# Kernel tuning notes

Measured on AMD Instinct MI355X. Metric: run time of the kernel, lower is better.

## Reference

```python
import jax, jax.numpy as jnp
import numpy as np

D_MODEL = 1024
EXPANSION = 4
NUM_TILES = 4
D_FF = D_MODEL * EXPANSION


def setup_inputs() -> dict:
    key = jax.random.key(0)
    k1, k2, k3, k4, k5 = jax.random.split(key, 5)
    x = jax.random.normal(k1, (8, 2048, D_MODEL), dtype=jnp.float32)
    w_up = jax.random.normal(k2, (D_FF, D_MODEL), dtype=jnp.float32) * 0.02
    b_up = jax.random.normal(k3, (D_FF,), dtype=jnp.float32) * 0.02
    w_down = jax.random.normal(k4, (D_MODEL, D_FF), dtype=jnp.float32) * 0.02
    b_down = jax.random.normal(k5, (D_MODEL,), dtype=jnp.float32) * 0.02
    return {"x": x, "w_up": w_up, "b_up": b_up, "w_down": w_down, "b_down": b_down}


def reference(x, w_up, b_up, w_down, b_down):
    B, T, C = x.shape
    xf = x.reshape(B * T, C)  # [N, d_model]
    N = B * T

    # Emergent tile signatures: sign of per-tile row sums of up_proj weight.
    tile_up = D_FF // NUM_TILES
    signatures = jnp.sign(w_up.reshape(NUM_TILES, tile_up, C).sum(axis=1))  # [num_tiles, d_model]

    # Routing: argmax over input-signature alignment -> one-hot gate.
    scores = xf @ signatures.T                      # [N, num_tiles]
    winner = jnp.argmax(scores, axis=-1)            # [N]
    gate = jax.nn.one_hot(winner, NUM_TILES, dtype=xf.dtype)  # [N, num_tiles]

    # Tile-gated up projection (gate scales output tile blocks), then ReLU.
    hidden = xf @ w_up.T + b_up                     # [N, d_ff]
    hidden = (hidden.reshape(N, NUM_TILES, tile_up) * gate[:, :, None]).reshape(N, D_FF)
    hidden = jax.nn.relu(hidden)

    # Tile-gated down projection.
    tile_down = D_MODEL // NUM_TILES
    out = hidden @ w_down.T + b_down                # [N, d_model]
    out = (out.reshape(N, NUM_TILES, tile_down) * gate[:, :, None]).reshape(N, D_MODEL)

    return out.reshape(B, T, D_MODEL), gate.reshape(B, T, NUM_TILES)
```

## Files before the change

### kernel.cpp

```cpp
#include <hip/hip_runtime.h>
#include <stdint.h>
#include <stddef.h>

#define N_TOK 16384
#define DM    1024
#define DFF   4096
#define NT    4
#define TU    1024
#define TD    256

typedef __attribute__((ext_vector_type(8))) short  short8;
typedef __attribute__((ext_vector_type(4))) short  short4v;
typedef __attribute__((ext_vector_type(4))) float  floatx4;

__device__ inline unsigned short f2bf(float f){
  union { float f; uint32_t u; } v; v.f = f;
  uint32_t u = v.u + 0x7FFFu + ((v.u >> 16) & 1u);
  return (unsigned short)(u >> 16);
}

__device__ __forceinline__ void gll16(const void* g, void* l){
  __builtin_amdgcn_global_load_lds(
      (const __attribute__((address_space(1))) unsigned int*)g,
      (__attribute__((address_space(3))) unsigned int*)l,
      16, 0, 0);
}

__global__ void k_sig_partial(const float* __restrict__ w_up,
                              float* __restrict__ partial,
                              unsigned short* __restrict__ wupb){
  const int b = blockIdx.x, tid = threadIdx.x;
  const int tile = b >> 6, chunk = b & 63;
  const int c0 = tid * 4;
  const int row0 = tile*TU + chunk*16;
  float s0=0.f, s1=0.f, s2=0.f, s3=0.f;
  const float* base = w_up + (size_t)row0 * DM + c0;
  #pragma unroll
  for (int r = 0; r < 16; ++r){
    floatx4 v = *(const floatx4*)(base + (size_t)r * DM);
    s0 += v[0]; s1 += v[1]; s2 += v[2]; s3 += v[3];
    short4v p;
    p[0]=(short)f2bf(v[0]); p[1]=(short)f2bf(v[1]);
    p[2]=(short)f2bf(v[2]); p[3]=(short)f2bf(v[3]);
    *(short4v*)(wupb + (size_t)(row0 + r) * DM + c0) = p;
  }
  float* p = partial + ((size_t)tile*DM + c0) * 64 + chunk;
  p[0] = s0; p[64] = s1; p[128] = s2; p[192] = s3;
}

__global__ void k_sig_final(const float* __restrict__ partial,
                            float* __restrict__ sig){
  const int g = blockIdx.x * 256 + threadIdx.x;
  const float* p = partial + (size_t)g * 64;
  float s = 0.f;
  #pragma unroll
  for (int i = 0; i < 64; ++i) s += p[i];
  sig[g] = (s > 0.f) ? 1.f : ((s < 0.f) ? -1.f : 0.f);
}

__global__ void k_wdown_conv(const float* __restrict__ w,
                             unsigned short* __restrict__ wb){
  const size_t i = ((size_t)blockIdx.x * 256 + threadIdx.x) * 8;
  floatx4 v0 = *(const floatx4*)(w + i);
  floatx4 v1 = *(const floatx4*)(w + i + 4);
  short8 p;
  p[0]=(short)f2bf(v0[0]); p[1]=(short)f2bf(v0[1]); p[2]=(short)f2bf(v0[2]); p[3]=(short)f2bf(v0[3]);
  p[4]=(short)f2bf(v1[0]); p[5]=(short)f2bf(v1[1]); p[6]=(short)f2bf(v1[2]); p[7]=(short)f2bf(v1[3]);
  *(short8*)(wb + i) = p;
}

__global__ __launch_bounds__(256) void k_route(
    const float* __restrict__ x, const float* __restrict__ sig,
    float* __restrict__ gate_out, int* __restrict__ winner,
    unsigned short* __restrict__ xbf){
  __shared__ float ssig[NT * DM];
  const int tid = threadIdx.x;
  for (int i = tid; i < NT*DM; i += 256) ssig[i] = sig[i];
  __syncthreads();
  const int wv = tid >> 6, lane = tid & 63;
  const int n = blockIdx.x * 4 + wv;
  const float* xr = x + (size_t)n * DM;
  unsigned short* xb = xbf + (size_t)n * 2048 + 1024;
  double a0=0.0, a1=0.0, a2=0.0, a3=0.0;
  #pragma unroll
  for (int j = 0; j < 4; ++j){
    const int c = j*256 + lane*4;
    floatx4 v = *(const floatx4*)(xr + c);
    short4v p;
    p[0]=(short)f2bf(v[0]); p[1]=(short)f2bf(v[1]);
    p[2]=(short)f2bf(v[2]); p[3]=(short)f2bf(v[3]);
    *(short4v*)(xb + c) = p;
    #pragma unroll
    for (int u = 0; u < 4; ++u){
      double xv = (double)v[u];
      a0 += xv * (double)ssig[c+u];
      a1 += xv * (double)ssig[DM   + c+u];
      a2 += xv * (double)ssig[2*DM + c+u];
      a3 += xv * (double)ssig[3*DM + c+u];
    }
  }
  #pragma unroll
  for (int off = 32; off > 0; off >>= 1){
    a0 += __shfl_down(a0, off, 64);
    a1 += __shfl_down(a1, off, 64);
    a2 += __shfl_down(a2, off, 64);
    a3 += __shfl_down(a3, off, 64);
  }
  if (lane == 0){
    double s[4] = {a0, a1, a2, a3};
    int w = 0;
    #pragma unroll
    for (int t = 1; t < 4; ++t) if (s[t] > s[w]) w = t;
    floatx4 g = { w==0 ? 1.f:0.f, w==1 ? 1.f:0.f, w==2 ? 1.f:0.f, w==3 ? 1.f:0.f };
    *(floatx4*)(gate_out + (size_t)n * 4) = g;
    winner[n] = w;
  }
}

__global__ void k_hist(const int* __restrict__ winner,
                       int* __restrict__ blk_cnt){
  __shared__ int wcnt[4][NT];
  const int tid = threadIdx.x, wv = tid >> 6, lane = tid & 63;
  const int w = winner[blockIdx.x * 256 + tid];
  #pragma unroll
  for (int t = 0; t < NT; ++t){
    unsigned long long m = __ballot(w == t);
    if (lane == 0) wcnt[wv][t] = __popcll(m);
  }
  __syncthreads();
  if (tid < NT){
    int s = wcnt[0][tid] + wcnt[1][tid] + wcnt[2][tid] + wcnt[3][tid];
    blk_cnt[blockIdx.x * NT + tid] = s;
  }
}

__global__ void k_scan(const int* __restrict__ blk_cnt,
                       int* __restrict__ meta, int* __restrict__ blk_base){
  __shared__ int s[256];
  const int tid = threadIdx.x;
  s[tid] = blk_cnt[tid];
  __syncthreads();
  if (tid == 0){
    int tot[NT] = {0,0,0,0};
    for (int b = 0; b < 64; ++b)
      for (int t = 0; t < NT; ++t) tot[t] += s[b*NT + t];
    int off = 0, base[NT];
    for (int t = 0; t < NT; ++t){ meta[t] = tot[t]; meta[4+t] = off; base[t] = off; off += tot[t]; }
    for (int b = 0; b < 64; ++b)
      for (int t = 0; t < NT; ++t){ int c = s[b*NT + t]; s[b*NT + t] = base[t]; base[t] += c; }
  }
  __syncthreads();
  blk_base[tid] = s[tid];
}

__global__ void k_scatter(const int* __restrict__ winner,
                          const int* __restrict__ blk_base,
                          int* __restrict__ idx){
  __shared__ int wcnt[4][NT];
  const int tid = threadIdx.x, wv = tid >> 6, lane = tid & 63;
  const int n = blockIdx.x * 256 + tid;
  const int w = winner[n];
  unsigned long long mymask = 0;
  #pragma unroll
  for (int t = 0; t < NT; ++t){
    unsigned long long m = __ballot(w == t);
    if (lane == 0) wcnt[wv][t] = __popcll(m);
    if (t == w) mymask = m;
  }
  __syncthreads();
  const unsigned long long below = (lane == 0) ? 0ull : (~0ull >> (64 - lane));
  int pos = blk_base[blockIdx.x * NT + w] + __popcll(mymask & below);
  for (int v = 0; v < wv; ++v) pos += wcnt[v][w];
  idx[pos] = n;
}

__global__ __launch_bounds__(256, 2) void k_gemm1(
    const unsigned short* __restrict__ xbf,
    const unsigned short* __restrict__ wupb,
    const float* __restrict__ b_up, const int* __restrict__ meta,
    const int* __restrict__ idx, unsigned short* __restrict__ hid){
  const int tile = blockIdx.z;
  const int cnt  = meta[tile];
  const int p0   = blockIdx.x * 128;
  if (p0 >= cnt) return;
  const int off  = meta[4 + tile];
  const int nb   = blockIdx.y;

  __shared__ unsigned short smem[24576];
  __shared__ int nrow[128];

  const int tid = threadIdx.x;
  if (tid < 128){
    int p = p0 + tid;
    nrow[tid] = idx[off + (p < cnt ? p : cnt - 1)];
  }
  __syncthreads();

  const int wv = tid >> 6, lane = tid & 63;
  const int wm = (wv >> 1) * 64, wn = (wv & 1) * 64;
  const int l16 = lane & 15, quad = lane >> 4;

  const int rsub = lane >> 2;
  const int kus  = (lane & 3) * 8;

  const int ra = wv*32 + rsub;
  const unsigned short* aptr0 = xbf + (size_t)nrow[ra]      * 2048 + 1024 + kus;
  const unsigned short* aptr1 = xbf + (size_t)nrow[ra + 16] * 2048 + 1024 + kus;
  const unsigned short* bptr0 = wupb + (size_t)(tile*TU + nb*128 + wv*32 + rsub) * DM + kus;
  const unsigned short* bptr1 = bptr0 + 16 * DM;

  floatx4 acc[4][4];
  #pragma unroll
  for (int i = 0; i < 4; ++i)
    #pragma unroll
    for (int j = 0; j < 4; ++j) acc[i][j] = (floatx4){0.f,0.f,0.f,0.f};

  auto stage = [&](int b, int s){
    unsigned short* d = smem + b*8192 + wv*1024;
    const int ko = s*32;
    gll16(aptr0 + ko, d);
    gll16(aptr1 + ko, d + 512);
    gll16(bptr0 + ko, d + 4096);
    gll16(bptr1 + ko, d + 4608);
  };

  auto compute = [&](int b){
    const unsigned short* A  = smem + b*8192;
    const unsigned short* Bp = A + 4096;
    short8 af[4], bfr[4];
    #pragma unroll
    for (int i = 0; i < 4; ++i) af[i]  = *(const short8*)(A  + (wm + i*16 + l16)*32 + quad*8);
    #pragma unroll
    for (int j = 0; j < 4; ++j) bfr[j] = *(const short8*)(Bp + (wn + j*16 + l16)*32 + quad*8);
    #pragma unroll
    for (int i = 0; i < 4; ++i)
      #pragma unroll
      for (int j = 0; j < 4; ++j)
        acc[i][j] = __builtin_amdgcn_mfma_f32_16x16x32_bf16(af[i], bfr[j], acc[i][j], 0, 0, 0);
  };

  stage(0, 0);
  stage(1, 1);

  #pragma unroll
  for (int s = 0; s < 32; ++s){
    if (s == 31) asm volatile("s_waitcnt vmcnt(0)" ::: "memory");
    else         asm volatile("s_waitcnt vmcnt(4)" ::: "memory");
    __builtin_amdgcn_s_barrier();
    __builtin_amdgcn_sched_barrier(0);
    if (s < 30) stage((s + 2) % 3, s + 2);
    compute(s % 3);
    __builtin_amdgcn_sched_barrier(0);
    asm volatile("" ::: "memory");
    __builtin_amdgcn_s_barrier();
  }

  const int gcol0 = nb*128;
  #pragma unroll
  for (int half = 0; half < 2; ++half){
    if ((wv >> 1) == half){
      #pragma unroll
      for (int i = 0; i < 4; ++i){
        #pragma unroll
        for (int j = 0; j < 4; ++j){
          const int col = wn + j*16 + l16;
          const float bias = b_up[tile*TU + gcol0 + col];
          #pragma unroll
          for (int r = 0; r < 4; ++r){
            const int lrow = i*16 + quad*4 + r;
            float v = acc[i][j][r] + bias;
            smem[lrow*136 + col] = f2bf(v > 0.f ? v : 0.f);
          }
        }
      }
    }
    __syncthreads();
    #pragma unroll
    for (int c = tid; c < 1024; c += 256){
      const int lrow = c >> 4, k8 = (c & 15) * 8;
      const int m = half*64 + lrow;
      if (p0 + m < cnt){
        short8 vv = *(const short8*)(smem + lrow*136 + k8);
        *(short8*)(hid + (size_t)nrow[m]*2048 + gcol0 + k8) = vv;
      }
    }
    __syncthreads();
  }
}

__global__ __launch_bounds__(256, 2) void k_gemm2(
    const unsigned short* __restrict__ hid,
    const unsigned short* __restrict__ wdownb,
    const float* __restrict__ b_down, const int* __restrict__ meta,
    const int* __restrict__ idx, float* __restrict__ out){
  const int tile = blockIdx.z;
  const int cnt  = meta[tile];
  const int p0   = blockIdx.x * 32;
  if (p0 >= cnt) return;
  const int off  = meta[4 + tile];

  __shared__ unsigned short smem[18432];
  unsigned short* As0 = smem;
  unsigned short* As1 = smem + 1024;
  unsigned short* Bs0 = smem + 2048;
  unsigned short* Bs1 = smem + 10240;
  float* epi = (float*)smem;
  __shared__ int nrow[32];

  const int tid = threadIdx.x;
  if (tid < 32){
    int p = p0 + tid;
    nrow[tid] = idx[off + (p < cnt ? p : cnt - 1)];
  }
  __syncthreads();

  const int wv = tid >> 6, lane = tid & 63;
  const int wn = wv * 64;
  const int l16 = lane & 15, quad = lane >> 4;

  const int rsub = lane >> 2;
  const int kus  = (lane & 3) * 8;

  const int arow = (wv & 1)*16 + rsub;
  const unsigned short* aptr = hid + (size_t)nrow[arow] * 2048 + kus;
  const int aoff = (wv >> 1) * 32;
  unsigned short* asd = (wv < 2 ? As0 : As1) + ((wv & 1)*16) * 32;
  const unsigned short* bptr = wdownb + (size_t)(tile*TD + wv*64 + rsub) * DFF + tile*TU + kus;
  unsigned short* bsd0 = Bs0 + (wv*64) * 32;
  unsigned short* bsd1 = Bs1 + (wv*64) * 32;

  floatx4 acc[2][4];
  #pragma unroll
  for (int i = 0; i < 2; ++i)
    #pragma unroll
    for (int j = 0; j < 4; ++j) acc[i][j] = (floatx4){0.f,0.f,0.f,0.f};

  for (int k0 = 0; k0 < TU; k0 += 64){
    gll16(aptr + k0 + aoff, asd);
    gll16(bptr + k0,               bsd0);
    gll16(bptr + k0 + 16*DFF,      bsd0 + 16*32);
    gll16(bptr + k0 + 32*DFF,      bsd0 + 32*32);
    gll16(bptr + k0 + 48*DFF,      bsd0 + 48*32);
    gll16(bptr + k0 + 32,          bsd1);
    gll16(bptr + k0 + 32 + 16*DFF, bsd1 + 16*32);
    gll16(bptr + k0 + 32 + 32*DFF, bsd1 + 32*32);
    gll16(bptr + k0 + 32 + 48*DFF, bsd1 + 48*32);
    __syncthreads();
    {
      short8 af[2], bfr[4];
      #pragma unroll
      for (int i = 0; i < 2; ++i) af[i]  = *(const short8*)(As0 + (i*16 + l16)*32 + quad*8);
      #pragma unroll
      for (int j = 0; j < 4; ++j) bfr[j] = *(const short8*)(Bs0 + (wn + j*16 + l16)*32 + quad*8);
      #pragma unroll
      for (int i = 0; i < 2; ++i)
        #pragma unroll
        for (int j = 0; j < 4; ++j)
          acc[i][j] = __builtin_amdgcn_mfma_f32_16x16x32_bf16(af[i], bfr[j], acc[i][j], 0, 0, 0);
    }
    {
      short8 af[2], bfr[4];
      #pragma unroll
      for (int i = 0; i < 2; ++i) af[i]  = *(const short8*)(As1 + (i*16 + l16)*32 + quad*8);
      #pragma unroll
      for (int j = 0; j < 4; ++j) bfr[j] = *(const short8*)(Bs1 + (wn + j*16 + l16)*32 + quad*8);
      #pragma unroll
      for (int i = 0; i < 2; ++i)
        #pragma unroll
        for (int j = 0; j < 4; ++j)
          acc[i][j] = __builtin_amdgcn_mfma_f32_16x16x32_bf16(af[i], bfr[j], acc[i][j], 0, 0, 0);
    }
    __syncthreads();
  }

  const floatx4 z4 = {0.f, 0.f, 0.f, 0.f};
  #pragma unroll
  for (int cb = 0; cb < 4; ++cb){
    if (cb == tile) continue;
    for (int c = tid; c < 32*64; c += 256){
      const int rowl = c >> 6, c4 = (c & 63) * 4;
      if (p0 + rowl < cnt)
        *(floatx4*)(out + (size_t)nrow[rowl]*DM + cb*256 + c4) = z4;
    }
  }

  #pragma unroll
  for (int half = 0; half < 2; ++half){
    #pragma unroll
    for (int j = 0; j < 4; ++j){
      const int col = wn + j*16 + l16;
      const float bias = b_down[tile*TD + col];
      #pragma unroll
      for (int r = 0; r < 4; ++r){
        const int lrow = quad*4 + r;
        epi[lrow*260 + col] = acc[half][j][r] + bias;
      }
    }
    __syncthreads();
    #pragma unroll
    for (int c = tid; c < 1024; c += 256){
      const int lrow = c >> 6, c4 = (c & 63) * 4;
      const int m = half*16 + lrow;
      if (p0 + m < cnt){
        floatx4 v = *(const floatx4*)(epi + lrow*260 + c4);
        *(floatx4*)(out + (size_t)nrow[m]*DM + tile*TD + c4) = v;
      }
    }
    __syncthreads();
  }
}

extern "C" void kernel_launch(void* const* d_in, const int* in_sizes, int n_in,
                              void* d_out, int out_size, void* d_ws, size_t ws_size,
                              hipStream_t stream){
  const float* x      = (const float*)d_in[0];
  const float* w_up   = (const float*)d_in[1];
  const float* b_up   = (const float*)d_in[2];
  const float* w_down = (const float*)d_in[3];
  const float* b_down = (const float*)d_in[4];

  unsigned short* wupb   = (unsigned short*)d_ws;
  unsigned short* wdownb = wupb + (size_t)DFF * DM;
  float* partial = (float*)(wdownb + (size_t)DM * DFF);
  float* sig     = partial + 262144;
  int*   ints    = (int*)(sig + 4096);
  int*   winner   = ints;
  int*   idx      = ints + 16384;
  int*   meta     = ints + 32768;
  int*   blk_cnt  = ints + 32776;
  int*   blk_base = ints + 33032;

  float*          out  = (float*)d_out;
  float*          gate = out + (size_t)N_TOK * DM;
  unsigned short* ob16 = (unsigned short*)d_out;

  k_sig_partial<<<dim3(NT*64), 256, 0, stream>>>(w_up, partial, wupb);
  k_sig_final  <<<dim3(16),    256, 0, stream>>>(partial, sig);
  k_wdown_conv <<<dim3(2048),  256, 0, stream>>>(w_down, wdownb);
  k_route      <<<dim3(N_TOK/4), 256, 0, stream>>>(x, sig, gate, winner, ob16);
  k_hist       <<<dim3(64),    256, 0, stream>>>(winner, blk_cnt);
  k_scan       <<<dim3(1),     256, 0, stream>>>(blk_cnt, meta, blk_base);
  k_scatter    <<<dim3(64),    256, 0, stream>>>(winner, blk_base, idx);
  k_gemm1      <<<dim3(128, 8, NT), 256, 0, stream>>>(ob16, wupb, b_up, meta, idx, ob16);
  k_gemm2      <<<dim3(512, 1, NT), 256, 0, stream>>>(ob16, wdownb, b_down, meta, idx, out);
}
```

Baseline: 276.9 us.

## Enlarge GEMM tiles to 256x256 with 512 threads and double gemm2 row tile

Gemm1 moves from a 128x128 tile with 256 threads and a 3-stage software pipeline to a 256x256 tile with 512 threads (8 waves, 128x64 per wave), loading 64-wide K chunks per synchronous step. Gemm2 doubles its row tile from 32 to 64 tokens, so each wave holds a 4x4 accumulator and the weight tile is reused across more rows. The aim is higher arithmetic intensity and less redundant global/LDS traffic. In exchange it drops the multi-stage prefetch pipeline in gemm1, which exposes load latency, raises register pressure with 32 accumulators per wave, and produces fewer blocks, so more of the wave slots can sit idle.

Result: slower. 301.5 us (+8.9%).

```diff
diff --git a/kernel.cpp b/kernel.cpp
--- a/kernel.cpp
+++ b/kernel.cpp
@@ -174,114 +174,107 @@
   idx[pos] = n;
 }
 
-__global__ __launch_bounds__(256, 2) void k_gemm1(
+__global__ __launch_bounds__(512, 2) void k_gemm1(
     const unsigned short* __restrict__ xbf,
     const unsigned short* __restrict__ wupb,
     const float* __restrict__ b_up, const int* __restrict__ meta,
     const int* __restrict__ idx, unsigned short* __restrict__ hid){
   const int tile = blockIdx.z;
   const int cnt  = meta[tile];
-  const int p0   = blockIdx.x * 128;
+  const int p0   = blockIdx.x * 256;
   if (p0 >= cnt) return;
   const int off  = meta[4 + tile];
-  const int nb   = blockIdx.y;
-
-  __shared__ unsigned short smem[24576];
-  __shared__ int nrow[128];
+  const int nbc  = blockIdx.y * 256;
+
+  __shared__ unsigned short smem[32768];
+  __shared__ int nrow[256];
 
   const int tid = threadIdx.x;
-  if (tid < 128){
+  if (tid < 256){
     int p = p0 + tid;
     nrow[tid] = idx[off + (p < cnt ? p : cnt - 1)];
   }
   __syncthreads();
 
   const int wv = tid >> 6, lane = tid & 63;
-  const int wm = (wv >> 1) * 64, wn = (wv & 1) * 64;
+  const int wr = wv >> 2, wc = wv & 3;
   const int l16 = lane & 15, quad = lane >> 4;
-
   const int rsub = lane >> 2;
   const int kus  = (lane & 3) * 8;
 
-  const int ra = wv*32 + rsub;
-  const unsigned short* aptr0 = xbf + (size_t)nrow[ra]      * 2048 + 1024 + kus;
-  const unsigned short* aptr1 = xbf + (size_t)nrow[ra + 16] * 2048 + 1024 + kus;
-  const unsigned short* bptr0 = wupb + (size_t)(tile*TU + nb*128 + wv*32 + rsub) * DM + kus;
+  const int sr = wv*32 + rsub;
+  const unsigned short* aptr0 = xbf + (size_t)nrow[sr]      * 2048 + 1024 + kus;
+  const unsigned short* aptr1 = xbf + (size_t)nrow[sr + 16] * 2048 + 1024 + kus;
+  const unsigned short* bptr0 = wupb + (size_t)(tile*TU + nbc + wv*32 + rsub) * DM + kus;
   const unsigned short* bptr1 = bptr0 + 16 * DM;
 
-  floatx4 acc[4][4];
-  #pragma unroll
-  for (int i = 0; i < 4; ++i)
+  unsigned short* const ad0 = smem + wv*1024;
+  unsigned short* const ad1 = ad0 + 8192;
+  unsigned short* const bd0 = ad0 + 16384;
+  unsigned short* const bd1 = ad0 + 24576;
+
+  floatx4 acc[8][4];
+  #pragma unroll
+  for (int i = 0; i < 8; ++i)
     #pragma unroll
     for (int j = 0; j < 4; ++j) acc[i][j] = (floatx4){0.f,0.f,0.f,0.f};
 
-  auto stage = [&](int b, int s){
-    unsigned short* d = smem + b*8192 + wv*1024;
-    const int ko = s*32;
-    gll16(aptr0 + ko, d);
-    gll16(aptr1 + ko, d + 512);
-    gll16(bptr0 + ko, d + 4096);
-    gll16(bptr1 + ko, d + 4608);
-  };
-
-  auto compute = [&](int b){
-    const unsigned short* A  = smem + b*8192;
-    const unsigned short* Bp = A + 4096;
-    short8 af[4], bfr[4];
-    #pragma unroll
-    for (int i = 0; i < 4; ++i) af[i]  = *(const short8*)(A  + (wm + i*16 + l16)*32 + quad*8);
-    #pragma unroll
-    for (int j = 0; j < 4; ++j) bfr[j] = *(const short8*)(Bp + (wn + j*16 + l16)*32 + quad*8);
-    #pragma unroll
-    for (int i = 0; i < 4; ++i)
+  for (int k0 = 0; k0 < DM; k0 += 64){
+    gll16(aptr0 + k0,      ad0);
+    gll16(aptr1 + k0,      ad0 + 512);
+    gll16(aptr0 + k0 + 32, ad1);
+    gll16(aptr1 + k0 + 32, ad1 + 512);
+    gll16(bptr0 + k0,      bd0);
+    gll16(bptr1 + k0,      bd0 + 512);
+    gll16(bptr0 + k0 + 32, bd1);
+    gll16(bptr1 + k0 + 32, bd1 + 512);
+    __syncthreads();
+    #pragma unroll
+    for (int c = 0; c < 2; ++c){
+      const unsigned short* A  = smem + c*8192;
+      const unsigned short* Bp = smem + 16384 + c*8192;
+      short8 bfr[4];
       #pragma unroll
       for (int j = 0; j < 4; ++j)
-        acc[i][j] = __builtin_amdgcn_mfma_f32_16x16x32_bf16(af[i], bfr[j], acc[i][j], 0, 0, 0);
-  };
-
-  stage(0, 0);
-  stage(1, 1);
-
-  #pragma unroll
-  for (int s = 0; s < 32; ++s){
-    if (s == 31) asm volatile("s_waitcnt vmcnt(0)" ::: "memory");
-    else         asm volatile("s_waitcnt vmcnt(4)" ::: "memory");
-    __builtin_amdgcn_s_barrier();
-    __builtin_amdgcn_sched_barrier(0);
-    if (s < 30) stage((s + 2) % 3, s + 2);
-    compute(s % 3);
-    __builtin_amdgcn_sched_barrier(0);
-    asm volatile("" ::: "memory");
-    __builtin_amdgcn_s_barrier();
-  }
-
-  const int gcol0 = nb*128;
-  #pragma unroll
-  for (int half = 0; half < 2; ++half){
-    if ((wv >> 1) == half){
-      #pragma unroll
-      for (int i = 0; i < 4; ++i){
+        bfr[j] = *(const short8*)(Bp + (wc*64 + j*16 + l16)*32 + quad*8);
+      #pragma unroll
+      for (int i = 0; i < 8; ++i){
+        short8 af = *(const short8*)(A + (wr*128 + i*16 + l16)*32 + quad*8);
+        #pragma unroll
+        for (int j = 0; j < 4; ++j)
+          acc[i][j] = __builtin_amdgcn_mfma_f32_16x16x32_bf16(af, bfr[j], acc[i][j], 0, 0, 0);
+      }
+    }
+    __syncthreads();
+  }
+
+  #pragma unroll
+  for (int p = 0; p < 4; ++p){
+    if (wr == (p >> 1)){
+      #pragma unroll
+      for (int ii = 0; ii < 4; ++ii){
+        const int i = (p & 1)*4 + ii;
         #pragma unroll
         for (int j = 0; j < 4; ++j){
-          const int col = wn + j*16 + l16;
-          const float bias = b_up[tile*TU + gcol0 + col];
+          const int col = wc*64 + j*16 + l16;
+          const float bias = b_up[tile*TU + nbc + col];
           #pragma unroll
           for (int r = 0; r < 4; ++r){
-            const int lrow = i*16 + quad*4 + r;
+            const int lrow = ii*16 + quad*4 + r;
             float v = acc[i][j][r] + bias;
-            smem[lrow*136 + col] = f2bf(v > 0.f ? v : 0.f);
+            smem[lrow*264 + col] = f2bf(v > 0.f ? v : 0.f);
           }
         }
       }
     }
     __syncthreads();
     #pragma unroll
-    for (int c = tid; c < 1024; c += 256){
-      const int lrow = c >> 4, k8 = (c & 15) * 8;
-      const int m = half*64 + lrow;
+    for (int c = tid; c < 2048; c += 512){
+      const int lrow = c >> 5, k8 = (c & 31) * 8;
+      const int m = p*64 + lrow;
       if (p0 + m < cnt){
-        short8 vv = *(const short8*)(smem + lrow*136 + k8);
-        *(short8*)(hid + (size_t)nrow[m]*2048 + gcol0 + k8) = vv;
+        short8 vv = *(const short8*)(smem + lrow*264 + k8);
+        *(short8*)(hid + (size_t)nrow[m]*2048 + nbc + k8) = vv;
       }
     }
     __syncthreads();
@@ -295,20 +288,16 @@
     const int* __restrict__ idx, float* __restrict__ out){
   const int tile = blockIdx.z;
   const int cnt  = meta[tile];
-  const int p0   = blockIdx.x * 32;
+  const int p0   = blockIdx.x * 64;
   if (p0 >= cnt) return;
   const int off  = meta[4 + tile];
 
-  __shared__ unsigned short smem[18432];
-  unsigned short* As0 = smem;
-  unsigned short* As1 = smem + 1024;
-  unsigned short* Bs0 = smem + 2048;
-  unsigned short* Bs1 = smem + 10240;
+  __shared__ unsigned short smem[20480];
   float* epi = (float*)smem;
-  __shared__ int nrow[32];
+  __shared__ int nrow[64];
 
   const int tid = threadIdx.x;
-  if (tid < 32){
+  if (tid < 64){
     int p = p0 + tid;
     nrow[tid] = idx[off + (p < cnt ? p : cnt - 1)];
   }
@@ -317,59 +306,49 @@
   const int wv = tid >> 6, lane = tid & 63;
   const int wn = wv * 64;
   const int l16 = lane & 15, quad = lane >> 4;
-
   const int rsub = lane >> 2;
   const int kus  = (lane & 3) * 8;
 
-  const int arow = (wv & 1)*16 + rsub;
-  const unsigned short* aptr = hid + (size_t)nrow[arow] * 2048 + kus;
-  const int aoff = (wv >> 1) * 32;
-  unsigned short* asd = (wv < 2 ? As0 : As1) + ((wv & 1)*16) * 32;
+  const unsigned short* aptr = hid + (size_t)nrow[wv*16 + rsub] * 2048 + kus;
+  unsigned short* const asd0 = smem + (wv*16) * 32;
+  unsigned short* const asd1 = asd0 + 2048;
   const unsigned short* bptr = wdownb + (size_t)(tile*TD + wv*64 + rsub) * DFF + tile*TU + kus;
-  unsigned short* bsd0 = Bs0 + (wv*64) * 32;
-  unsigned short* bsd1 = Bs1 + (wv*64) * 32;
-
-  floatx4 acc[2][4];
-  #pragma unroll
-  for (int i = 0; i < 2; ++i)
+  unsigned short* const bsd0 = smem + 4096  + (wv*64) * 32;
+  unsigned short* const bsd1 = bsd0 + 8192;
+
+  floatx4 acc[4][4];
+  #pragma unroll
+  for (int i = 0; i < 4; ++i)
     #pragma unroll
     for (int j = 0; j < 4; ++j) acc[i][j] = (floatx4){0.f,0.f,0.f,0.f};
 
   for (int k0 = 0; k0 < TU; k0 += 64){
-    gll16(aptr + k0 + aoff, asd);
+    gll16(aptr + k0,      asd0);
+    gll16(aptr + k0 + 32, asd1);
     gll16(bptr + k0,               bsd0);
-    gll16(bptr + k0 + 16*DFF,      bsd0 + 16*32);
-    gll16(bptr + k0 + 32*DFF,      bsd0 + 32*32);
-    gll16(bptr + k0 + 48*DFF,      bsd0 + 48*32);
+    gll16(bptr + k0 + 16*DFF,      bsd0 + 512);
+    gll16(bptr + k0 + 32*DFF,      bsd0 + 1024);
+    gll16(bptr + k0 + 48*DFF,      bsd0 + 1536);
     gll16(bptr + k0 + 32,          bsd1);
-    gll16(bptr + k0 + 32 + 16*DFF, bsd1 + 16*32);
-    gll16(bptr + k0 + 32 + 32*DFF, bsd1 + 32*32);
-    gll16(bptr + k0 + 32 + 48*DFF, bsd1 + 48*32);
-    __syncthreads();
-    {
-      short8 af[2], bfr[4];
-      #pragma unroll
-      for (int i = 0; i < 2; ++i) af[i]  = *(const short8*)(As0 + (i*16 + l16)*32 + quad*8);
-      #pragma unroll
-      for (int j = 0; j < 4; ++j) bfr[j] = *(const short8*)(Bs0 + (wn + j*16 + l16)*32 + quad*8);
-      #pragma unroll
-      for (int i = 0; i < 2; ++i)
+    gll16(bptr + k0 + 32 + 16*DFF, bsd1 + 512);
+    gll16(bptr + k0 + 32 + 32*DFF, bsd1 + 1024);
+    gll16(bptr + k0 + 32 + 48*DFF, bsd1 + 1536);
+    __syncthreads();
+    #pragma unroll
+    for (int c = 0; c < 2; ++c){
+      const unsigned short* A  = smem + c*2048;
+      const unsigned short* Bp = smem + 4096 + c*8192;
+      short8 af[4], bfr[4];
+      #pragma unroll
+      for (int i = 0; i < 4; ++i) af[i]  = *(const short8*)(A  + (i*16 + l16)*32 + quad*8);
+      #pragma unroll
+      for (int j = 0; j < 4; ++j) bfr[j] = *(const short8*)(Bp + (wn + j*16 + l16)*32 + quad*8);
+      #pragma unroll
+      for (int i = 0; i < 4; ++i)
         #pragma unroll
         for (int j = 0; j < 4; ++j)
           acc[i][j] = __builtin_amdgcn_mfma_f32_16x16x32_bf16(af[i], bfr[j], acc[i][j], 0, 0, 0);
     }
-    {
-      short8 af[2], bfr[4];
-      #pragma unroll
-      for (int i = 0; i < 2; ++i) af[i]  = *(const short8*)(As1 + (i*16 + l16)*32 + quad*8);
-      #pragma unroll
-      for (int j = 0; j < 4; ++j) bfr[j] = *(const short8*)(Bs1 + (wn + j*16 + l16)*32 + quad*8);
-      #pragma unroll
-      for (int i = 0; i < 2; ++i)
-        #pragma unroll
-        for (int j = 0; j < 4; ++j)
-          acc[i][j] = __builtin_amdgcn_mfma_f32_16x16x32_bf16(af[i], bfr[j], acc[i][j], 0, 0, 0);
-    }
     __syncthreads();
   }
 
@@ -377,7 +356,7 @@
   #pragma unroll
   for (int cb = 0; cb < 4; ++cb){
     if (cb == tile) continue;
-    for (int c = tid; c < 32*64; c += 256){
+    for (int c = tid; c < 64*64; c += 256){
       const int rowl = c >> 6, c4 = (c & 63) * 4;
       if (p0 + rowl < cnt)
         *(floatx4*)(out + (size_t)nrow[rowl]*DM + cb*256 + c4) = z4;
@@ -385,22 +364,26 @@
   }
 
   #pragma unroll
-  for (int half = 0; half < 2; ++half){
-    #pragma unroll
-    for (int j = 0; j < 4; ++j){
-      const int col = wn + j*16 + l16;
-      const float bias = b_down[tile*TD + col];
-      #pragma unroll
-      for (int r = 0; r < 4; ++r){
-        const int lrow = quad*4 + r;
-        epi[lrow*260 + col] = acc[half][j][r] + bias;
+  for (int h = 0; h < 2; ++h){
+    #pragma unroll
+    for (int ii = 0; ii < 2; ++ii){
+      const int i = h*2 + ii;
+      #pragma unroll
+      for (int j = 0; j < 4; ++j){
+        const int col = wn + j*16 + l16;
+        const float bias = b_down[tile*TD + col];
+        #pragma unroll
+        for (int r = 0; r < 4; ++r){
+          const int lrow = ii*16 + quad*4 + r;
+          epi[lrow*260 + col] = acc[i][j][r] + bias;
+        }
       }
     }
     __syncthreads();
     #pragma unroll
-    for (int c = tid; c < 1024; c += 256){
+    for (int c = tid; c < 2048; c += 256){
       const int lrow = c >> 6, c4 = (c & 63) * 4;
-      const int m = half*16 + lrow;
+      const int m = h*32 + lrow;
       if (p0 + m < cnt){
         floatx4 v = *(const floatx4*)(epi + lrow*260 + c4);
         *(floatx4*)(out + (size_t)nrow[m]*DM + tile*TD + c4) = v;
@@ -441,6 +424,6 @@
   k_hist       <<<dim3(64),    256, 0, stream>>>(winner, blk_cnt);
   k_scan       <<<dim3(1),     256, 0, stream>>>(blk_cnt, meta, blk_base);
   k_scatter    <<<dim3(64),    256, 0, stream>>>(winner, blk_base, idx);
-  k_gemm1      <<<dim3(128, 8, NT), 256, 0, stream>>>(ob16, wupb, b_up, meta, idx, ob16);
-  k_gemm2      <<<dim3(512, 1, NT), 256, 0, stream>>>(ob16, wdownb, b_down, meta, idx, out);
-}
+  k_gemm1      <<<dim3(64, 4, NT), 512, 0, stream>>>(ob16, wupb, b_up, meta, idx, ob16);
+  k_gemm2      <<<dim3(256, 1, NT), 256, 0, stream>>>(ob16, wdownb, b_down, meta, idx, out);
+}
```
